# Performance work log

Measured on AMD Instinct MI355X. Metric: run time of the kernel, lower is better.

Reference implementation:

```python
import jax, jax.numpy as jnp
import numpy as np

# Per-channel block sizes (init arg). [0,1] rows are identity channels.
BLOCK_SIZES = np.array(
    [[0, 1]] * 2 + [[1, 1]] * 2 + [[2, 2]] * 4 + [[4, 4]] * 4 + [[3, 3]] * 4
)


def _groups():
    """Static grouping: unique non-identity block sizes -> channel index arrays."""
    out = []
    for b in np.unique(BLOCK_SIZES, axis=0):
        if 0 in b:
            continue  # identity channels: passed through untouched
        ch = np.where(np.all(BLOCK_SIZES == b, axis=1))[0]
        out.append(((int(b[0]), int(b[1])), ch))
    return out


GROUPS = _groups()


def setup_inputs() -> dict:
    key = jax.random.key(0)
    activation = jax.random.normal(key, (32, 16, 224, 224), dtype=jnp.float32)
    return {"activation": activation}


def reference(activation) -> jnp.ndarray:
    N, C, H, W = activation.shape
    relu_map = jnp.ones_like(activation)
    for (bh, bw), ch in GROUPS:
        cur = activation[:, ch]                      # [N, Cg, H, W] channel gather
        ph, pw = (-H) % bh, (-W) % bw                # pad to block multiples
        cur = jnp.pad(cur, ((0, 0), (0, 0), (0, ph), (0, pw)))
        Hp, Wp = H + ph, W + pw
        Cg = cur.shape[1]
        # space-to-depth block sum (sum sign == mean sign)
        s = cur.reshape(N, Cg, Hp // bh, bh, Wp // bw, bw).sum(axis=(3, 5))
        sign = (s >= 0).astype(activation.dtype)     # DReLU on block sum
        # broadcast sign back over each block (depth-to-space) and unpad
        m = jnp.broadcast_to(
            sign[:, :, :, None, :, None], (N, Cg, Hp // bh, bh, Wp // bw, bw)
        ).reshape(N, Cg, Hp, Wp)[:, :, :H, :W]
        relu_map = relu_map.at[:, ch].set(m)         # channel scatter
    # identity channels keep relu_map == 1, so a single multiply is faithful
    return activation * relu_map
```

## Files before the change

kernel.cpp:

```cpp
#include <hip/hip_runtime.h>

#define HW      224
#define PLANE   50176
#define NSTRIDE 802816

constexpr int A_END = 1605632;
constexpr int B_END = A_END + 802816;
constexpr int C_END = B_END + 401408;
constexpr int TOTAL = C_END + 720000;

__global__ __launch_bounds__(256) void blockrelu_kernel(
    const float* __restrict__ in, float* __restrict__ out) {
  const int tid = blockIdx.x * 256 + threadIdx.x;
  if (tid >= TOTAL) return;

  if (tid < A_END) {
    int n = tid / PLANE;
    int r = tid - n * PLANE;
    int c = r / 12544;
    long off = (long)n * NSTRIDE + (long)r * 4;
    float4 v = *(const float4*)(in + off);
    if (c >= 2) {
      v.x = (v.x >= 0.f) ? v.x : 0.f;
      v.y = (v.y >= 0.f) ? v.y : 0.f;
      v.z = (v.z >= 0.f) ? v.z : 0.f;
      v.w = (v.w >= 0.f) ? v.w : 0.f;
    }
    *(float4*)(out + off) = v;
  } else if (tid < B_END) {
    int u = tid - A_END;
    int n = u / 25088;
    int v2 = u - n * 25088;
    int c = 4 + v2 / 6272;
    int w2 = v2 % 6272;
    int brow = w2 / 56;
    int rcol = w2 - brow * 56;
    long base = (long)n * NSTRIDE + (long)c * PLANE + (long)(2 * brow) * HW + 4 * rcol;
    float4 a = *(const float4*)(in + base);
    float4 b = *(const float4*)(in + base + HW);
    float s0 = ((a.x + a.y) + b.x) + b.y;
    float s1 = ((a.z + a.w) + b.z) + b.w;
    if (s0 < 0.f) { a.x = 0.f; a.y = 0.f; b.x = 0.f; b.y = 0.f; }
    if (s1 < 0.f) { a.z = 0.f; a.w = 0.f; b.z = 0.f; b.w = 0.f; }
    *(float4*)(out + base) = a;
    *(float4*)(out + base + HW) = b;
  } else if (tid < C_END) {
    int u = tid - B_END;
    int n = u / 12544;
    int v2 = u - n * 12544;
    int c = 8 + v2 / 3136;
    int w2 = v2 % 3136;
    int by = w2 / 56;
    int bx = w2 - by * 56;
    long base = (long)n * NSTRIDE + (long)c * PLANE + (long)(4 * by) * HW + 4 * bx;
    float4 r0 = *(const float4*)(in + base);
    float4 r1 = *(const float4*)(in + base + HW);
    float4 r2 = *(const float4*)(in + base + 2 * HW);
    float4 r3 = *(const float4*)(in + base + 3 * HW);
    float s = r0.x; s += r0.y; s += r0.z; s += r0.w;
    s += r1.x; s += r1.y; s += r1.z; s += r1.w;
    s += r2.x; s += r2.y; s += r2.z; s += r2.w;
    s += r3.x; s += r3.y; s += r3.z; s += r3.w;
    if (s < 0.f) {
      r0 = make_float4(0.f, 0.f, 0.f, 0.f);
      r1 = r0; r2 = r0; r3 = r0;
    }
    *(float4*)(out + base) = r0;
    *(float4*)(out + base + HW) = r1;
    *(float4*)(out + base + 2 * HW) = r2;
    *(float4*)(out + base + 3 * HW) = r3;
  } else {
    int u = tid - C_END;
    int n = u / 22500;
    int v2 = u - n * 22500;
    int c = 12 + v2 / 5625;
    int w2 = v2 % 5625;
    int by = w2 / 75;
    int bx = w2 - by * 75;
    int h0 = 3 * by, w0 = 3 * bx;
    int hmax = (224 - h0 < 3) ? (224 - h0) : 3;
    int wmax = (224 - w0 < 3) ? (224 - w0) : 3;
    long base = (long)n * NSTRIDE + (long)c * PLANE + (long)h0 * HW + w0;
    float vals[3][3];
    float s = 0.f;
    #pragma unroll
    for (int i = 0; i < 3; ++i) {
      #pragma unroll
      for (int j = 0; j < 3; ++j) {
        float x = 0.f;
        if (i < hmax && j < wmax) x = in[base + i * HW + j];
        vals[i][j] = x;
        s += x;
      }
    }
    const float keep = (s >= 0.f) ? 1.f : 0.f;
    #pragma unroll
    for (int i = 0; i < 3; ++i) {
      #pragma unroll
      for (int j = 0; j < 3; ++j) {
        if (i < hmax && j < wmax) out[base + i * HW + j] = keep * vals[i][j];
      }
    }
  }
}

extern "C" void kernel_launch(void* const* d_in, const int* in_sizes, int n_in,
                              void* d_out, int out_size, void* d_ws, size_t ws_size,
                              hipStream_t stream) {
  const float* act = (const float*)d_in[0];
  float* out = (float*)d_out;
  const int grid = (TOTAL + 255) / 256;
  blockrelu_kernel<<<grid, 256, 0, stream>>>(act, out);
}
```

Measured before the change: 182.3 us.

## Stage 3x3 block-ReLU channels through LDS strips with vectorized loads

Replaces the per-thread scalar 3x3 gather for the block-3 channels with workgroups that load 9-row strips of a plane into shared memory using coalesced float4 loads. Block sums and masks are computed from LDS, then the strip is written back with float4 stores. The grid is reorganized by block ranges so each path is workgroup-uniform. This adds shared memory and barriers, and the static LDS allocation applies to all blocks, which could lower occupancy on the simple paths.

New measurement: 181.8 us. About the same (-0.3%).

```diff
diff --git a/kernel.cpp b/kernel.cpp
--- a/kernel.cpp
+++ b/kernel.cpp
@@ -4,17 +4,22 @@
 #define PLANE   50176
 #define NSTRIDE 802816
 
-constexpr int A_END = 1605632;
-constexpr int B_END = A_END + 802816;
-constexpr int C_END = B_END + 401408;
-constexpr int TOTAL = C_END + 720000;
+constexpr int A_BLOCKS = 6272;
+constexpr int AB   = A_BLOCKS;
+constexpr int ABC  = AB + 3136;
+constexpr int ABCD = ABC + 1568;
+constexpr int TOTAL_BLOCKS = ABCD + 3200;
 
 __global__ __launch_bounds__(256) void blockrelu_kernel(
     const float* __restrict__ in, float* __restrict__ out) {
-  const int tid = blockIdx.x * 256 + threadIdx.x;
-  if (tid >= TOTAL) return;
+  const int bid = blockIdx.x;
+  const int t = threadIdx.x;
 
-  if (tid < A_END) {
+  __shared__ float tile[9][228];
+  __shared__ float maskL[3][76];
+
+  if (bid < AB) {
+    int tid = bid * 256 + t;
     int n = tid / PLANE;
     int r = tid - n * PLANE;
     int c = r / 12544;
@@ -27,8 +32,8 @@
       v.w = (v.w >= 0.f) ? v.w : 0.f;
     }
     *(float4*)(out + off) = v;
-  } else if (tid < B_END) {
-    int u = tid - A_END;
+  } else if (bid < ABC) {
+    int u = (bid - AB) * 256 + t;
     int n = u / 25088;
     int v2 = u - n * 25088;
     int c = 4 + v2 / 6272;
@@ -44,8 +49,8 @@
     if (s1 < 0.f) { a.z = 0.f; a.w = 0.f; b.z = 0.f; b.w = 0.f; }
     *(float4*)(out + base) = a;
     *(float4*)(out + base + HW) = b;
-  } else if (tid < C_END) {
-    int u = tid - B_END;
+  } else if (bid < ABCD) {
+    int u = (bid - ABC) * 256 + t;
     int n = u / 12544;
     int v2 = u - n * 12544;
     int c = 8 + v2 / 3136;
@@ -70,36 +75,52 @@
     *(float4*)(out + base + 2 * HW) = r2;
     *(float4*)(out + base + 3 * HW) = r3;
   } else {
-    int u = tid - C_END;
-    int n = u / 22500;
-    int v2 = u - n * 22500;
-    int c = 12 + v2 / 5625;
-    int w2 = v2 % 5625;
-    int by = w2 / 75;
-    int bx = w2 - by * 75;
-    int h0 = 3 * by, w0 = 3 * bx;
-    int hmax = (224 - h0 < 3) ? (224 - h0) : 3;
-    int wmax = (224 - w0 < 3) ? (224 - w0) : 3;
-    long base = (long)n * NSTRIDE + (long)c * PLANE + (long)h0 * HW + w0;
-    float vals[3][3];
-    float s = 0.f;
-    #pragma unroll
-    for (int i = 0; i < 3; ++i) {
+    int wg = bid - ABCD;
+    int p = wg / 25;
+    int sg = wg - p * 25;
+    int n = p >> 2;
+    int c = 12 + (p & 3);
+    int h0 = sg * 9;
+    int rows = (224 - h0 >= 9) ? 9 : (224 - h0);
+    long pbase = (long)n * NSTRIDE + (long)c * PLANE;
+
+    for (int i = t; i < 9 * 228; i += 256) ((float*)tile)[i] = 0.f;
+    __syncthreads();
+
+    const int nvec = rows * 56;
+    for (int idx = t; idx < nvec; idx += 256) {
+      int r = idx / 56;
+      int q = idx - r * 56;
+      float4 v = *(const float4*)(in + pbase + (long)(h0 + r) * HW + q * 4);
+      *(float4*)&tile[r][q * 4] = v;
+    }
+    __syncthreads();
+
+    if (t < 225) {
+      int br = t / 75;
+      int bx = t - br * 75;
+      int r0 = br * 3, c0 = bx * 3;
+      float s = 0.f;
       #pragma unroll
-      for (int j = 0; j < 3; ++j) {
-        float x = 0.f;
-        if (i < hmax && j < wmax) x = in[base + i * HW + j];
-        vals[i][j] = x;
-        s += x;
-      }
+      for (int i = 0; i < 3; ++i)
+        #pragma unroll
+        for (int j = 0; j < 3; ++j)
+          s += tile[r0 + i][c0 + j];
+      maskL[br][bx] = (s >= 0.f) ? 1.f : 0.f;
     }
-    const float keep = (s >= 0.f) ? 1.f : 0.f;
-    #pragma unroll
-    for (int i = 0; i < 3; ++i) {
-      #pragma unroll
-      for (int j = 0; j < 3; ++j) {
-        if (i < hmax && j < wmax) out[base + i * HW + j] = keep * vals[i][j];
-      }
+    __syncthreads();
+
+    for (int idx = t; idx < nvec; idx += 256) {
+      int r = idx / 56;
+      int q = idx - r * 56;
+      int col = q * 4;
+      float4 v = *(const float4*)&tile[r][col];
+      int br = r / 3;
+      v.x *= maskL[br][(col    ) / 3];
+      v.y *= maskL[br][(col + 1) / 3];
+      v.z *= maskL[br][(col + 2) / 3];
+      v.w *= maskL[br][(col + 3) / 3];
+      *(float4*)(out + pbase + (long)(h0 + r) * HW + col) = v;
     }
   }
 }
@@ -109,6 +130,5 @@
                               hipStream_t stream) {
   const float* act = (const float*)d_in[0];
   float* out = (float*)d_out;
-  const int grid = (TOTAL + 255) / 256;
-  blockrelu_kernel<<<grid, 256, 0, stream>>>(act, out);
+  blockrelu_kernel<<<TOTAL_BLOCKS, 256, 0, stream>>>(act, out);
 }
```
